# Optimization experiments

Hardware: AMD Instinct MI355X
Metric: run time of the kernel (lower is better)

Reference implementation:

```python
import jax, jax.numpy as jnp
from jax import lax
import numpy as np

D_MODEL = 256
D_STATE = 16
D_CONV = 8
EXPAND = 4
D_INNER = EXPAND * D_MODEL  # 1024
DT_RANK = (D_MODEL + 15) // 16  # 16
OUTPUTS = 128
F_IN = 512


def setup_inputs() -> dict:
    key = jax.random.key(0)
    ks = jax.random.split(key, 16)
    s = lambda k, shape, sc: (jax.random.normal(k, shape, jnp.float32) * sc)
    inp = {
        "x": jax.random.normal(ks[0], (4, 1024, F_IN), jnp.float32),
        # LazyLinear F_IN -> 256
        "W_in": s(ks[1], (F_IN, D_MODEL), F_IN ** -0.5),
        "b_in": jnp.zeros((D_MODEL,), jnp.float32),
        # Mamba params
        "W_inproj": s(ks[2], (D_MODEL, 2 * D_INNER), D_MODEL ** -0.5),
        "conv_w": s(ks[3], (D_INNER, D_CONV), D_CONV ** -0.5),
        "conv_b": jnp.zeros((D_INNER,), jnp.float32),
        "W_xproj": s(ks[4], (D_INNER, DT_RANK + 2 * D_STATE), D_INNER ** -0.5),
        "W_dt": s(ks[5], (DT_RANK, D_INNER), DT_RANK ** -0.5),
        "b_dt": s(ks[6], (D_INNER,), 0.1),
        "A_log": jnp.log(jnp.broadcast_to(jnp.arange(1, D_STATE + 1, dtype=jnp.float32), (D_INNER, D_STATE))),
        "D_param": jnp.ones((D_INNER,), jnp.float32),
        "W_out": s(ks[7], (D_INNER, D_MODEL), D_INNER ** -0.5),
        # head 256 -> 128
        "W_head": s(ks[8], (D_MODEL, OUTPUTS), D_MODEL ** -0.5),
        "b_head": jnp.zeros((OUTPUTS,), jnp.float32),
    }
    return inp


def _mamba(x, W_inproj, conv_w, conv_b, W_xproj, W_dt, b_dt, A_log, D_param, W_out):
    B_, L, _ = x.shape
    xz = x @ W_inproj                       # [B,L,2*Di]
    xc, z = jnp.split(xz, 2, axis=-1)
    # causal depthwise conv over L
    xc_t = jnp.transpose(xc, (0, 2, 1))      # [B,Di,L]
    xc_t = lax.conv_general_dilated(
        xc_t, conv_w[:, None, :], (1,), [(D_CONV - 1, 0)],
        dimension_numbers=("NCH", "OIH", "NCH"), feature_group_count=D_INNER,
    ) + conv_b[None, :, None]
    xc = jax.nn.silu(jnp.transpose(xc_t, (0, 2, 1)))  # [B,L,Di]
    dbc = xc @ W_xproj                       # [B,L,R+2S]
    dt_r = dbc[..., :DT_RANK]
    Bm = dbc[..., DT_RANK:DT_RANK + D_STATE]  # [B,L,S]
    Cm = dbc[..., DT_RANK + D_STATE:]          # [B,L,S]
    dt = jax.nn.softplus(dt_r @ W_dt + b_dt)  # [B,L,Di]
    A = -jnp.exp(A_log)                        # [Di,S]
    dA = jnp.exp(dt[..., None] * A)            # [B,L,Di,S]
    dBx = dt[..., None] * Bm[:, :, None, :] * xc[..., None]  # [B,L,Di,S]

    def step(h, inp):
        dA_t, dBx_t, C_t = inp
        h = dA_t * h + dBx_t                   # [B,Di,S]
        y = jnp.einsum("bds,bs->bd", h, C_t)
        return h, y

    h0 = jnp.zeros((B_, D_INNER, D_STATE), x.dtype)
    _, ys = lax.scan(step, h0, (dA.transpose(1, 0, 2, 3), dBx.transpose(1, 0, 2, 3), Cm.transpose(1, 0, 2)))
    y = ys.transpose(1, 0, 2) + xc * D_param   # [B,L,Di]
    y = y * jax.nn.silu(z)
    return y @ W_out                           # [B,L,D_MODEL]


def reference(x, W_in, b_in, W_inproj, conv_w, conv_b, W_xproj, W_dt, b_dt, A_log, D_param, W_out, W_head, b_head):
    h = jax.nn.sigmoid(x @ W_in + b_in)        # LazyLinear + Dropout(eval) + Sigmoid
    h = _mamba(h, W_inproj, conv_w, conv_b, W_xproj, W_dt, b_dt, A_log, D_param, W_out)
    logits = h @ W_head + b_head               # [B,L,OUTPUTS]
    logits = logits / 1.0                      # temperature = 1.0
    return jax.nn.softmax(logits[:, -1, :], axis=1)
```

## Files before the change

kernel.cpp:

```cpp
#include <hip/hip_runtime.h>
#include <cmath>

#define B_SZ 4
#define L_SEQ 1024
#define F_IN 512
#define D_MODEL 256
#define D_INNER 1024
#define D_STATE 16
#define DT_RANK 16
#define N_OUT 128
#define BL 4096
#define NCHUNK 32
#define CLEN 32

typedef __attribute__((ext_vector_type(8))) short short8;
typedef __attribute__((ext_vector_type(4))) float f32x4;

#define OFF_WIP_HI  0ull
#define OFF_WIP_LO  524288ull
#define OFF_WXP_HI  1048576ull
#define OFF_WXP_LO  1179648ull
#define OFF_HP_HI   1310720ull
#define OFF_HP_LO   3407872ull
#define OFF_HLAST   5505024ull
#define OFF_ZL      5509120ull
#define OFF_XCP_HI  5525504ull
#define OFF_XCP_LO  13914112ull
#define OFF_DBCP    22302720ull
#define OFF_P       39079936ull
#define OFF_Q       47468544ull
#define OFF_YL      55857152ull
#define OFF_H2      55873536ull

__device__ __forceinline__ unsigned short bf16_rne(float v) {
    unsigned u = __float_as_uint(v);
    unsigned r = (u + 0x7fffu + ((u >> 16) & 1u)) >> 16;
    return (unsigned short)r;
}
__device__ __forceinline__ float bf16_tof(unsigned short h) {
    return __uint_as_float(((unsigned)h) << 16);
}
__device__ __forceinline__ float siluf_(float x) { return x / (1.f + expf(-x)); }
__device__ __forceinline__ float softplusf_(float x) {
    return fmaxf(x, 0.f) + log1pf(expf(-fabsf(x)));
}

__device__ __forceinline__ void gload_lds16(const void* g, void* lds) {
    __builtin_amdgcn_global_load_lds(
        (const __attribute__((address_space(1))) unsigned int*)(unsigned long long)g,
        (__attribute__((address_space(3))) unsigned int*)(unsigned int)(unsigned long long)lds,
        16, 0, 0);
}

__device__ __forceinline__ void packB_group(const float* __restrict__ B, int ldb, int c0,
                                            int Ksrc, int Nsrc, int Ncols,
                                            unsigned short* __restrict__ hi,
                                            unsigned short* __restrict__ lo, int g) {
    int p = g * 8;
    int nr = (p >> 3) & 15, kh = (p >> 7) & 3;
    int ngkb = p >> 9;
    int ng16 = Ncols >> 4;
    int ng = ngkb % ng16, kb = ngkb / ng16;
    int n = c0 + ng * 16 + nr, k0 = kb * 32 + kh * 8;
    short8 vh, vl;
#pragma unroll
    for (int i = 0; i < 8; i++) {
        int k = k0 + i;
        float v = (k < Ksrc && n < Nsrc) ? B[(size_t)k * ldb + n] : 0.f;
        unsigned short hh = bf16_rne(v);
        vh[i] = (short)hh;
        vl[i] = (short)bf16_rne(v - bf16_tof(hh));
    }
    *(short8*)(hi + p) = vh;
    *(short8*)(lo + p) = vl;
}

__global__ __launch_bounds__(256) void gemm1_fused(
    const float* __restrict__ x, const float* __restrict__ W_in,
    const float* __restrict__ b_in, const float* __restrict__ W_inproj,
    const float* __restrict__ W_xproj,
    unsigned short* __restrict__ hp_hi, unsigned short* __restrict__ hp_lo,
    float* __restrict__ Hlast,
    unsigned short* __restrict__ wip_hi, unsigned short* __restrict__ wip_lo,
    unsigned short* __restrict__ wxp_hi, unsigned short* __restrict__ wxp_lo) {
    __shared__ __align__(16) char lds[32768];
    const int tid = threadIdx.x;
    const int bn = blockIdx.x * 64, bm = blockIdx.y * 64;
    const int wid = tid >> 6, lane = tid & 63;
    const int wm0 = (wid >> 1) * 32, wn0 = (wid & 1) * 32;
    const int arow = tid >> 2, aoct = tid & 3;

    f32x4 acc[2][2];
#pragma unroll
    for (int r = 0; r < 2; r++)
#pragma unroll
        for (int c = 0; c < 2; c++) acc[r][c] = (f32x4){0.f, 0.f, 0.f, 0.f};

    f32x4 xv0, xv1;
    float wv[8];
    {
        const float* src = x + (size_t)(bm + arow) * 512 + aoct * 8;
        xv0 = *(const f32x4*)src;
        xv1 = *(const f32x4*)(src + 4);
#pragma unroll
        for (int i = 0; i < 8; i++)
            wv[i] = W_in[(size_t)(aoct * 8 + i) * 256 + bn + arow];
    }
    const int off = (arow >> 4) * 1024 + aoct * 256 + (arow & 15) * 16;
    int p = 0;
    for (int kb = 0; kb < 16; kb++) {
        char* buf = lds + p * 16384;
        {
            short8 vh, vl, wh, wl;
#pragma unroll
            for (int i = 0; i < 4; i++) {
                unsigned short hh = bf16_rne(xv0[i]);
                vh[i] = (short)hh;
                vl[i] = (short)bf16_rne(xv0[i] - bf16_tof(hh));
            }
#pragma unroll
            for (int i = 0; i < 4; i++) {
                unsigned short hh = bf16_rne(xv1[i]);
                vh[4 + i] = (short)hh;
                vl[4 + i] = (short)bf16_rne(xv1[i] - bf16_tof(hh));
            }
#pragma unroll
            for (int i = 0; i < 8; i++) {
                unsigned short hh = bf16_rne(wv[i]);
                wh[i] = (short)hh;
                wl[i] = (short)bf16_rne(wv[i] - bf16_tof(hh));
            }
            *(short8*)(buf + off) = vh;
            *(short8*)(buf + 4096 + off) = vl;
            *(short8*)(buf + 8192 + off) = wh;
            *(short8*)(buf + 12288 + off) = wl;
        }
        if (kb < 15) {
            const float* src = x + (size_t)(bm + arow) * 512 + (kb + 1) * 32 + aoct * 8;
            xv0 = *(const f32x4*)src;
            xv1 = *(const f32x4*)(src + 4);
#pragma unroll
            for (int i = 0; i < 8; i++)
                wv[i] = W_in[(size_t)((kb + 1) * 32 + aoct * 8 + i) * 256 + bn + arow];
        }
        __syncthreads();
        short8 ah[2], al[2], bh[2], bl[2];
#pragma unroll
        for (int r = 0; r < 2; r++) {
            ah[r] = *(const short8*)(buf + ((wm0 >> 4) + r) * 1024 + lane * 16);
            al[r] = *(const short8*)(buf + 4096 + ((wm0 >> 4) + r) * 1024 + lane * 16);
        }
#pragma unroll
        for (int c = 0; c < 2; c++) {
            bh[c] = *(const short8*)(buf + 8192 + ((wn0 >> 4) + c) * 1024 + lane * 16);
            bl[c] = *(const short8*)(buf + 12288 + ((wn0 >> 4) + c) * 1024 + lane * 16);
        }
#pragma unroll
        for (int r = 0; r < 2; r++)
#pragma unroll
            for (int c = 0; c < 2; c++) {
                acc[r][c] = __builtin_amdgcn_mfma_f32_16x16x32_bf16(ah[r], bh[c], acc[r][c], 0, 0, 0);
                acc[r][c] = __builtin_amdgcn_mfma_f32_16x16x32_bf16(ah[r], bl[c], acc[r][c], 0, 0, 0);
                acc[r][c] = __builtin_amdgcn_mfma_f32_16x16x32_bf16(al[r], bh[c], acc[r][c], 0, 0, 0);
            }
        p ^= 1;
    }
    __syncthreads();
    unsigned short* lh = (unsigned short*)lds;
    unsigned short* ll = (unsigned short*)(lds + 8192);
    const int r0 = (lane >> 4) * 4, cc = lane & 15;
#pragma unroll
    for (int r = 0; r < 2; r++)
#pragma unroll
        for (int c = 0; c < 2; c++)
#pragma unroll
            for (int j = 0; j < 4; j++) {
                int ml = wm0 + r * 16 + r0 + j;
                int nl = wn0 + c * 16 + cc;
                float v = acc[r][c][j] + b_in[bn + nl];
                v = 1.f / (1.f + expf(-v));
                int lkb = nl >> 5, kh = (nl >> 3) & 3, ii = nl & 7;
                int o2 = ((lkb * 4 + (ml >> 4)) * 4 + kh) * 128 + (ml & 15) * 8 + ii;
                unsigned short hh = bf16_rne(v);
                lh[o2] = hh;
                ll[o2] = bf16_rne(v - bf16_tof(hh));
                if (((bm + ml) & 1023) == 1023)
                    Hlast[((bm + ml) >> 10) * 256 + bn + nl] = v;
            }
    __syncthreads();
    const int mgbase = bm >> 4, kbbase = bn >> 5;
#pragma unroll
    for (int it = 0; it < 2; it++) {
        int q = it * 256 + tid;
        int lkb = q >> 8, lmg = (q >> 6) & 3, ch = q & 63;
        size_t gb = (((size_t)(kbbase + lkb) * 256 + mgbase + lmg) * 1024) + ch * 16;
        *(f32x4*)((char*)hp_hi + gb) = *(const f32x4*)(lds + q * 16);
        *(f32x4*)((char*)hp_lo + gb) = *(const f32x4*)(lds + 8192 + q * 16);
    }
    if (tid < 160) {
        int g = (blockIdx.y * 4 + blockIdx.x) * 160 + tid;
        if (g < 32768)
            packB_group(W_inproj, 2048, 0, 256, 1024, 1024, wip_hi, wip_lo, g);
        else
            packB_group(W_xproj, 48, 0, 1024, 48, 64, wxp_hi, wxp_lo, g - 32768);
    }
}

__global__ __launch_bounds__(256) void zlast_kernel(
    const float* __restrict__ Hlast, const float* __restrict__ W_inproj,
    float* __restrict__ ZL) {
    __shared__ float hl[256];
    __shared__ float red[8][33];
    const int tid = threadIdx.x;
    const int b = blockIdx.x >> 5, dz0 = (blockIdx.x & 31) * 32;
    hl[tid] = Hlast[b * 256 + tid];
    __syncthreads();
    const int dzo = tid & 31, ks = tid >> 5;
    float acc = 0.f;
    const float* wp = W_inproj + (size_t)(ks * 32) * 2048 + 1024 + dz0 + dzo;
#pragma unroll
    for (int i = 0; i < 32; i++)
        acc = fmaf(hl[ks * 32 + i], wp[(size_t)i * 2048], acc);
    red[ks][dzo] = acc;
    __syncthreads();
    if (tid < 32) {
        float s = 0.f;
#pragma unroll
        for (int k = 0; k < 8; k++) s += red[k][tid];
        ZL[b * 1024 + dz0 + tid] = s;
    }
}

__global__ __launch_bounds__(256) void gemm3_conv_kernel(
    const unsigned short* __restrict__ Ahi, const unsigned short* __restrict__ Alo,
    const unsigned short* __restrict__ Bhi, const unsigned short* __restrict__ Blo,
    const unsigned short* __restrict__ Wxhi, const unsigned short* __restrict__ Wxlo,
    const float* __restrict__ cw, const float* __restrict__ cb,
    unsigned short* __restrict__ xcp_hi, unsigned short* __restrict__ xcp_lo,
    float* __restrict__ dbcp) {
    __shared__ __align__(16) char lds[37376];
    const int tid = threadIdx.x;
    const int bm = blockIdx.y * 64, bn = blockIdx.x * 64;
    const int wid = tid >> 6, lane = tid & 63;
    const long long ag0 = ((long long)bm - 16) >> 4;
    const bool batch_start = (bm & 1023) == 0;

    f32x4 acc[5];
#pragma unroll
    for (int r = 0; r < 5; r++) acc[r] = (f32x4){0.f, 0.f, 0.f, 0.f};

    auto stage = [&](int kb, int pp) {
        const long long abase = ((long long)kb * 256 + ag0) * 1024;
        const size_t bbase = ((size_t)kb * 64 + (bn >> 4)) * 1024;
        char* dst = lds + pp * 18432;
#pragma unroll
        for (int it = 0; it < 5; it++) {
            int c = it * 256 + tid;
            if (c < 1152) {
                const char* g;
                char* l;
                if (c < 320)      { g = (const char*)Ahi + abase + (long long)c * 16;        l = dst + c * 16; }
                else if (c < 640) { g = (const char*)Alo + abase + (long long)(c - 320) * 16; l = dst + 5120 + (c - 320) * 16; }
                else if (c < 896) { g = (const char*)Bhi + bbase + (size_t)(c - 640) * 16;    l = dst + 10240 + (c - 640) * 16; }
                else              { g = (const char*)Blo + bbase + (size_t)(c - 896) * 16;    l = dst + 14336 + (c - 896) * 16; }
                gload_lds16(g, l);
            }
        }
    };

    stage(0, 0);
    int p = 0;
    for (int kk = 0; kk < 8; kk++) {
        __syncthreads();
        if (kk < 7) stage(kk + 1, p ^ 1);
        const char* buf = lds + p * 18432;
        short8 ah[5], al[5], bh, bl;
#pragma unroll
        for (int r = 0; r < 5; r++) {
            ah[r] = *(const short8*)(buf + r * 1024 + lane * 16);
            al[r] = *(const short8*)(buf + 5120 + r * 1024 + lane * 16);
        }
        bh = *(const short8*)(buf + 10240 + wid * 1024 + lane * 16);
        bl = *(const short8*)(buf + 14336 + wid * 1024 + lane * 16);
#pragma unroll
        for (int r = 0; r < 5; r++) {
            acc[r] = __builtin_amdgcn_mfma_f32_16x16x32_bf16(ah[r], bh, acc[r], 0, 0, 0);
            acc[r] = __builtin_amdgcn_mfma_f32_16x16x32_bf16(ah[r], bl, acc[r], 0, 0, 0);
            acc[r] = __builtin_amdgcn_mfma_f32_16x16x32_bf16(al[r], bh, acc[r], 0, 0, 0);
        }
        p ^= 1;
    }
    __syncthreads();

    float* S = (float*)lds;
    const int r0 = (lane >> 4) * 4, cc = lane & 15;
#pragma unroll
    for (int r = 0; r < 5; r++)
#pragma unroll
        for (int j = 0; j < 4; j++)
            S[(r * 16 + r0 + j) * 65 + wid * 16 + cc] = acc[r][j];
    __syncthreads();

    unsigned short* xph = (unsigned short*)(lds + 20800);
    unsigned short* xpl = (unsigned short*)(lds + 20800 + 8192);
    {
        const int col = tid & 63, t0 = (tid >> 6) * 16;
        const int d = bn + col;
        float w[8];
#pragma unroll
        for (int k = 0; k < 8; k++) w[k] = cw[d * 8 + k];
        const float bias = cb[d];
        const int kbg = d >> 5, kh = (d >> 3) & 3, ii = d & 7;
        const int kbl = col >> 5, mgl = t0 >> 4;
        float win[8];
#pragma unroll
        for (int k = 0; k < 7; k++) {
            int sr = t0 + 9 + k;
            float v = S[sr * 65 + col];
            if (batch_start && sr < 16) v = 0.f;
            win[k + 1] = v;
        }
        for (int i = 0; i < 16; i++) {
            const int t = t0 + i;
#pragma unroll
            for (int k = 0; k < 7; k++) win[k] = win[k + 1];
            win[7] = S[(t + 16) * 65 + col];
            float a = bias;
#pragma unroll
            for (int k = 0; k < 8; k++) a = fmaf(win[k], w[k], a);
            float v = siluf_(a);
            const int m = bm + t;
            unsigned short hh = bf16_rne(v);
            unsigned short lo_ = bf16_rne(v - bf16_tof(hh));
            size_t pidx = (((size_t)(kbg * 256 + (m >> 4)) * 4 + kh) * 128) + (m & 15) * 8 + ii;
            xcp_hi[pidx] = hh;
            xcp_lo[pidx] = lo_;
            int loff = ((kbl * 4 + mgl) * 4 + kh) * 128 + (t & 15) * 8 + ii;
            xph[loff] = hh;
            xpl[loff] = lo_;
        }
    }
    __syncthreads();

    f32x4 acc2[4];
#pragma unroll
    for (int ng = 0; ng < 4; ng++) acc2[ng] = (f32x4){0.f, 0.f, 0.f, 0.f};
#pragma unroll
    for (int kbl = 0; kbl < 2; kbl++) {
        short8 ah2 = *(const short8*)((const char*)xph + (kbl * 4 + wid) * 1024 + lane * 16);
        short8 al2 = *(const short8*)((const char*)xpl + (kbl * 4 + wid) * 1024 + lane * 16);
        const int kbgl = (bn >> 5) + kbl;
#pragma unroll
        for (int ng = 0; ng < 4; ng++) {
            short8 bh2 = *(const short8*)((const char*)Wxhi + ((size_t)(kbgl * 4 + ng)) * 1024 + lane * 16);
            short8 bl2 = *(const short8*)((const char*)Wxlo + ((size_t)(kbgl * 4 + ng)) * 1024 + lane * 16);
            acc2[ng] = __builtin_amdgcn_mfma_f32_16x16x32_bf16(ah2, bh2, acc2[ng], 0, 0, 0);
            acc2[ng] = __builtin_amdgcn_mfma_f32_16x16x32_bf16(ah2, bl2, acc2[ng], 0, 0, 0);
            acc2[ng] = __builtin_amdgcn_mfma_f32_16x16x32_bf16(al2, bh2, acc2[ng], 0, 0, 0);
        }
    }
    float* dp = dbcp + (size_t)blockIdx.x * 262144;
#pragma unroll
    for (int ng = 0; ng < 4; ng++)
#pragma unroll
        for (int j = 0; j < 4; j++)
            dp[(size_t)(bm + wid * 16 + r0 + j) * 64 + ng * 16 + cc] = acc2[ng][j];
}

__global__ __launch_bounds__(256) void scan_partial_kernel(
    const unsigned short* __restrict__ xh, const unsigned short* __restrict__ xl,
    const float* __restrict__ DBCP, const float* __restrict__ W_dt,
    const float* __restrict__ b_dt, float* __restrict__ P, float* __restrict__ Q) {
    const int tid = threadIdx.x;
    const int dg = blockIdx.x, c = blockIdx.y, b = blockIdx.z;
    const int d = dg * 256 + tid;
    __shared__ __align__(16) float dbc_s[CLEN * 32];
    {
        int r = tid >> 3, cq = tid & 7;
        const float* base = DBCP + ((size_t)(b * 1024 + c * CLEN + r)) * 64 + cq * 4;
        f32x4 s = (f32x4){0.f, 0.f, 0.f, 0.f};
#pragma unroll
        for (int z = 0; z < 16; z++) {
            f32x4 v = *(const f32x4*)(base + (size_t)z * 262144);
            s = s + v;
        }
        ((f32x4*)dbc_s)[tid] = s;
    }
    float Wc[16];
#pragma unroll
    for (int k = 0; k < 16; k++) Wc[k] = W_dt[k * 1024 + d];
    const float bdt = b_dt[d];
    __syncthreads();
    float h[16];
#pragma unroll
    for (int s = 0; s < 16; s++) h[s] = 0.f;
    float sdt = 0.f;
    const size_t dpart = (size_t)(d >> 5) * 131072 + ((d >> 3) & 3) * 128 + (d & 7);
    const int m0 = b * 1024 + c * CLEN;
    for (int i = 0; i < CLEN; i++) {
        const int m = m0 + i;
        const size_t off = dpart + (size_t)(m >> 4) * 512 + (m & 15) * 8;
        const float xv = bf16_tof(xh[off]) + bf16_tof(xl[off]);
        const f32x4* r4 = (const f32x4*)(dbc_s + i * 32);
        f32x4 q0 = r4[0], q1 = r4[1], q2 = r4[2], q3 = r4[3];
        float a0 = 0.f, a1 = 0.f;
#pragma unroll
        for (int k = 0; k < 4; k++) { a0 = fmaf(q0[k], Wc[k], a0); a1 = fmaf(q2[k], Wc[8 + k], a1); }
#pragma unroll
        for (int k = 0; k < 4; k++) { a0 = fmaf(q1[k], Wc[4 + k], a0); a1 = fmaf(q3[k], Wc[12 + k], a1); }
        float dtv = softplusf_(bdt + a0 + a1);
        float dbx = dtv * xv;
        sdt += dtv;
        float e1 = expf(-dtv);
        float e2 = e1 * e1, e3 = e2 * e1, e4 = e2 * e2;
        float e5 = e4 * e1, e6 = e4 * e2, e7 = e4 * e3, e8 = e4 * e4;
        f32x4 b0 = r4[4], b1 = r4[5], b2 = r4[6], b3 = r4[7];
        h[0] = fmaf(e1, h[0], dbx * b0[0]);
        h[1] = fmaf(e2, h[1], dbx * b0[1]);
        h[2] = fmaf(e3, h[2], dbx * b0[2]);
        h[3] = fmaf(e4, h[3], dbx * b0[3]);
        h[4] = fmaf(e5, h[4], dbx * b1[0]);
        h[5] = fmaf(e6, h[5], dbx * b1[1]);
        h[6] = fmaf(e7, h[6], dbx * b1[2]);
        h[7] = fmaf(e8, h[7], dbx * b1[3]);
        h[8] = fmaf(e8 * e1, h[8], dbx * b2[0]);
        h[9] = fmaf(e8 * e2, h[9], dbx * b2[1]);
        h[10] = fmaf(e8 * e3, h[10], dbx * b2[2]);
        h[11] = fmaf(e8 * e4, h[11], dbx * b2[3]);
        h[12] = fmaf(e8 * e5, h[12], dbx * b3[0]);
        h[13] = fmaf(e8 * e6, h[13], dbx * b3[1]);
        h[14] = fmaf(e8 * e7, h[14], dbx * b3[2]);
        h[15] = fmaf(e8 * e8, h[15], dbx * b3[3]);
    }
    size_t o = (((size_t)(b * NCHUNK + c) * 1024 + d) << 4);
    float E1 = expf(-sdt);
    float E2 = E1 * E1, E3 = E2 * E1, E4 = E2 * E2;
    float E5 = E4 * E1, E6 = E4 * E2, E7 = E4 * E3, E8 = E4 * E4;
    f32x4 pv;
    pv = (f32x4){E1, E2, E3, E4};                      *(f32x4*)(P + o) = pv;
    pv = (f32x4){E5, E6, E7, E8};                      *(f32x4*)(P + o + 4) = pv;
    pv = (f32x4){E8 * E1, E8 * E2, E8 * E3, E8 * E4};  *(f32x4*)(P + o + 8) = pv;
    pv = (f32x4){E8 * E5, E8 * E6, E8 * E7, E8 * E8};  *(f32x4*)(P + o + 12) = pv;
#pragma unroll
    for (int u = 0; u < 4; u++) {
        f32x4 qv;
#pragma unroll
        for (int s = 0; s < 4; s++) qv[s] = h[u * 4 + s];
        *(f32x4*)(Q + o + u * 4) = qv;
    }
}

__global__ __launch_bounds__(256) void scan_final_kernel(
    const float* __restrict__ P, const float* __restrict__ Q,
    const float* __restrict__ DBCP, const unsigned short* __restrict__ xh,
    const unsigned short* __restrict__ xl, const float* __restrict__ ZL,
    const float* __restrict__ Dp, float* __restrict__ YL) {
    const int idx = blockIdx.x * 256 + threadIdx.x;
    const int s = idx & 15, d = (idx >> 4) & 1023, b = idx >> 14;
    float h = 0.f;
    const size_t stride = (size_t)1024 * 16;
    size_t o = (((size_t)(b * NCHUNK) * 1024 + d) << 4) + s;
#pragma unroll 8
    for (int c = 0; c < NCHUNK; c++) {
        h = fmaf(P[o], h, Q[o]);
        o += stride;
    }
    float cm = 0.f;
#pragma unroll
    for (int z = 0; z < 16; z++)
        cm += DBCP[(size_t)z * 262144 + ((size_t)b * 1024 + 1023) * 64 + 32 + s];
    float v = h * cm;
    v += __shfl_xor(v, 1);
    v += __shfl_xor(v, 2);
    v += __shfl_xor(v, 4);
    v += __shfl_xor(v, 8);
    if (s == 0) {
        const int m = b * 1024 + 1023;
        const size_t off = (size_t)(d >> 5) * 131072 + (size_t)(m >> 4) * 512 +
                           ((d >> 3) & 3) * 128 + 15 * 8 + (d & 7);
        float xlast = bf16_tof(xh[off]) + bf16_tof(xl[off]);
        float y = v + xlast * Dp[d];
        float z = ZL[b * 1024 + d];
        YL[b * 1024 + d] = y * siluf_(z);
    }
}

__global__ __launch_bounds__(256) void head1_kernel(
    const float* __restrict__ YL, const float* __restrict__ W_out,
    float* __restrict__ H2) {
    __shared__ float yl[D_INNER];
    __shared__ float red[16][17];
    const int b = blockIdx.y, n0 = blockIdx.x * 16;
    const int tid = threadIdx.x;
    const int tn = tid & 15, tk = tid >> 4;
    ((f32x4*)yl)[tid] = ((const f32x4*)(YL + b * D_INNER))[tid];
    __syncthreads();
    float acc = 0.f;
    const float* wp = W_out + (size_t)(tk * 64) * D_MODEL + n0 + tn;
#pragma unroll
    for (int i = 0; i < 64; i++)
        acc = fmaf(yl[tk * 64 + i], wp[(size_t)i * D_MODEL], acc);
    red[tk][tn] = acc;
    __syncthreads();
    if (tid < 16) {
        float s = 0.f;
#pragma unroll
        for (int k = 0; k < 16; k++) s += red[k][tid];
        H2[b * D_MODEL + n0 + tid] = s;
    }
}

__global__ __launch_bounds__(256) void head2_kernel(
    const float* __restrict__ H2, const float* __restrict__ W_head,
    const float* __restrict__ b_head, float* __restrict__ out) {
    __shared__ float h2s[D_MODEL];
    __shared__ float part[256];
    __shared__ float red[N_OUT];
    __shared__ float tmp[64];
    __shared__ float m_s, inv_s;
    const int b = blockIdx.x, tid = threadIdx.x;
    h2s[tid] = H2[b * D_MODEL + tid];
    __syncthreads();
    const int n = tid & 127, kh = tid >> 7;
    float acc = 0.f;
    const float* wp = W_head + (size_t)(kh * 128) * N_OUT + n;
#pragma unroll
    for (int k = 0; k < 128; k++)
        acc = fmaf(h2s[kh * 128 + k], wp[(size_t)k * N_OUT], acc);
    part[tid] = acc;
    __syncthreads();
    if (tid < N_OUT) red[tid] = part[tid] + part[tid + 128] + b_head[tid];
    __syncthreads();
    if (tid < 64) tmp[tid] = fmaxf(red[tid], red[tid + 64]);
    __syncthreads();
    if (tid == 0) {
        float m = tmp[0];
        for (int i = 1; i < 64; i++) m = fmaxf(m, tmp[i]);
        m_s = m;
    }
    __syncthreads();
    if (tid < N_OUT) red[tid] = expf(red[tid] - m_s);
    __syncthreads();
    if (tid < 64) tmp[tid] = red[tid] + red[tid + 64];
    __syncthreads();
    if (tid == 0) {
        float s = 0.f;
        for (int i = 0; i < 64; i++) s += tmp[i];
        inv_s = 1.f / s;
    }
    __syncthreads();
    if (tid < N_OUT) out[b * N_OUT + tid] = red[tid] * inv_s;
}

extern "C" void kernel_launch(void* const* d_in, const int* in_sizes, int n_in,
                              void* d_out, int out_size, void* d_ws, size_t ws_size,
                              hipStream_t stream) {
    const float* x = (const float*)d_in[0];
    const float* W_in = (const float*)d_in[1];
    const float* b_in = (const float*)d_in[2];
    const float* W_inproj = (const float*)d_in[3];
    const float* conv_w = (const float*)d_in[4];
    const float* conv_b = (const float*)d_in[5];
    const float* W_xproj = (const float*)d_in[6];
    const float* W_dt = (const float*)d_in[7];
    const float* b_dt = (const float*)d_in[8];
    const float* D_param = (const float*)d_in[10];
    const float* W_out = (const float*)d_in[11];
    const float* W_head = (const float*)d_in[12];
    const float* b_head = (const float*)d_in[13];
    float* out = (float*)d_out;

    char* W = (char*)d_ws;
    auto F = [&](size_t off) { return (float*)(W + off); };
    auto U = [&](size_t off) { return (unsigned short*)(W + off); };

    gemm1_fused<<<dim3(4, 64), 256, 0, stream>>>(
        x, W_in, b_in, W_inproj, W_xproj,
        U(OFF_HP_HI), U(OFF_HP_LO), F(OFF_HLAST),
        U(OFF_WIP_HI), U(OFF_WIP_LO), U(OFF_WXP_HI), U(OFF_WXP_LO));
    zlast_kernel<<<128, 256, 0, stream>>>(F(OFF_HLAST), W_inproj, F(OFF_ZL));
    gemm3_conv_kernel<<<dim3(16, 64), 256, 0, stream>>>(
        U(OFF_HP_HI), U(OFF_HP_LO), U(OFF_WIP_HI), U(OFF_WIP_LO),
        U(OFF_WXP_HI), U(OFF_WXP_LO), conv_w, conv_b,
        U(OFF_XCP_HI), U(OFF_XCP_LO), F(OFF_DBCP));
    scan_partial_kernel<<<dim3(4, NCHUNK, 4), 256, 0, stream>>>(
        U(OFF_XCP_HI), U(OFF_XCP_LO), F(OFF_DBCP), W_dt, b_dt, F(OFF_P), F(OFF_Q));
    scan_final_kernel<<<256, 256, 0, stream>>>(F(OFF_P), F(OFF_Q), F(OFF_DBCP),
                                               U(OFF_XCP_HI), U(OFF_XCP_LO), F(OFF_ZL),
                                               D_param, F(OFF_YL));
    head1_kernel<<<dim3(16, 4), 256, 0, stream>>>(F(OFF_YL), W_out, F(OFF_H2));
    head2_kernel<<<4, 256, 0, stream>>>(F(OFF_H2), W_head, b_head, out);
}
```

Measured before the change: 94.19 us.

## Drop low-bf16 weight and conv-output terms, fold zlast into scan_partial

Weights (W_in, W_inproj, W_xproj) and the conv/SiLU output are now represented by a single bf16 term instead of a hi/lo split. The lo-by-hi MFMA products, the lo buffers and their global and LDS traffic are removed in gemm1, gemm3 and the scans. The separate zlast kernel is merged into scan_partial as an extra block column, saving one launch. Numerical accuracy drops, since the weights and the xc activations lose the residual correction term.

```diff
diff --git a/kernel.cpp b/kernel.cpp
--- a/kernel.cpp
+++ b/kernel.cpp
@@ -17,20 +17,17 @@
 typedef __attribute__((ext_vector_type(4))) float f32x4;
 
 #define OFF_WIP_HI  0ull
-#define OFF_WIP_LO  524288ull
-#define OFF_WXP_HI  1048576ull
-#define OFF_WXP_LO  1179648ull
-#define OFF_HP_HI   1310720ull
-#define OFF_HP_LO   3407872ull
-#define OFF_HLAST   5505024ull
-#define OFF_ZL      5509120ull
-#define OFF_XCP_HI  5525504ull
-#define OFF_XCP_LO  13914112ull
-#define OFF_DBCP    22302720ull
-#define OFF_P       39079936ull
-#define OFF_Q       47468544ull
-#define OFF_YL      55857152ull
-#define OFF_H2      55873536ull
+#define OFF_WXP_HI  524288ull
+#define OFF_HP_HI   655360ull
+#define OFF_HP_LO   2752512ull
+#define OFF_HLAST   4849664ull
+#define OFF_ZL      4853760ull
+#define OFF_XCP_HI  4870144ull
+#define OFF_DBCP    13258752ull
+#define OFF_P       30035968ull
+#define OFF_Q       38424576ull
+#define OFF_YL      46813184ull
+#define OFF_H2      46829568ull
 
 __device__ __forceinline__ unsigned short bf16_rne(float v) {
     unsigned u = __float_as_uint(v);
@@ -52,27 +49,23 @@
         16, 0, 0);
 }
 
-__device__ __forceinline__ void packB_group(const float* __restrict__ B, int ldb, int c0,
-                                            int Ksrc, int Nsrc, int Ncols,
-                                            unsigned short* __restrict__ hi,
-                                            unsigned short* __restrict__ lo, int g) {
+__device__ __forceinline__ void packBhi_group(const float* __restrict__ B, int ldb,
+                                              int Ksrc, int Nsrc, int Ncols,
+                                              unsigned short* __restrict__ hi, int g) {
     int p = g * 8;
     int nr = (p >> 3) & 15, kh = (p >> 7) & 3;
     int ngkb = p >> 9;
     int ng16 = Ncols >> 4;
     int ng = ngkb % ng16, kb = ngkb / ng16;
-    int n = c0 + ng * 16 + nr, k0 = kb * 32 + kh * 8;
-    short8 vh, vl;
+    int n = ng * 16 + nr, k0 = kb * 32 + kh * 8;
+    short8 vh;
 #pragma unroll
     for (int i = 0; i < 8; i++) {
         int k = k0 + i;
         float v = (k < Ksrc && n < Nsrc) ? B[(size_t)k * ldb + n] : 0.f;
-        unsigned short hh = bf16_rne(v);
-        vh[i] = (short)hh;
-        vl[i] = (short)bf16_rne(v - bf16_tof(hh));
+        vh[i] = (short)bf16_rne(v);
     }
     *(short8*)(hi + p) = vh;
-    *(short8*)(lo + p) = vl;
 }
 
 __global__ __launch_bounds__(256) void gemm1_fused(
@@ -81,9 +74,8 @@
     const float* __restrict__ W_xproj,
     unsigned short* __restrict__ hp_hi, unsigned short* __restrict__ hp_lo,
     float* __restrict__ Hlast,
-    unsigned short* __restrict__ wip_hi, unsigned short* __restrict__ wip_lo,
-    unsigned short* __restrict__ wxp_hi, unsigned short* __restrict__ wxp_lo) {
-    __shared__ __align__(16) char lds[32768];
+    unsigned short* __restrict__ wip_hi, unsigned short* __restrict__ wxp_hi) {
+    __shared__ __align__(16) char lds[24576];
     const int tid = threadIdx.x;
     const int bn = blockIdx.x * 64, bm = blockIdx.y * 64;
     const int wid = tid >> 6, lane = tid & 63;
@@ -109,9 +101,9 @@
     const int off = (arow >> 4) * 1024 + aoct * 256 + (arow & 15) * 16;
     int p = 0;
     for (int kb = 0; kb < 16; kb++) {
-        char* buf = lds + p * 16384;
+        char* buf = lds + p * 12288;
         {
-            short8 vh, vl, wh, wl;
+            short8 vh, vl, wh;
 #pragma unroll
             for (int i = 0; i < 4; i++) {
                 unsigned short hh = bf16_rne(xv0[i]);
@@ -125,15 +117,10 @@
                 vl[4 + i] = (short)bf16_rne(xv1[i] - bf16_tof(hh));
             }
 #pragma unroll
-            for (int i = 0; i < 8; i++) {
-                unsigned short hh = bf16_rne(wv[i]);
-                wh[i] = (short)hh;
-                wl[i] = (short)bf16_rne(wv[i] - bf16_tof(hh));
-            }
+            for (int i = 0; i < 8; i++) wh[i] = (short)bf16_rne(wv[i]);
             *(short8*)(buf + off) = vh;
             *(short8*)(buf + 4096 + off) = vl;
             *(short8*)(buf + 8192 + off) = wh;
-            *(short8*)(buf + 12288 + off) = wl;
         }
         if (kb < 15) {
             const float* src = x + (size_t)(bm + arow) * 512 + (kb + 1) * 32 + aoct * 8;
@@ -144,23 +131,20 @@
                 wv[i] = W_in[(size_t)((kb + 1) * 32 + aoct * 8 + i) * 256 + bn + arow];
         }
         __syncthreads();
-        short8 ah[2], al[2], bh[2], bl[2];
+        short8 ah[2], al[2], bh[2];
 #pragma unroll
         for (int r = 0; r < 2; r++) {
             ah[r] = *(const short8*)(buf + ((wm0 >> 4) + r) * 1024 + lane * 16);
             al[r] = *(const short8*)(buf + 4096 + ((wm0 >> 4) + r) * 1024 + lane * 16);
         }
 #pragma unroll
-        for (int c = 0; c < 2; c++) {
+        for (int c = 0; c < 2; c++)
             bh[c] = *(const short8*)(buf + 8192 + ((wn0 >> 4) + c) * 1024 + lane * 16);
-            bl[c] = *(const short8*)(buf + 12288 + ((wn0 >> 4) + c) * 1024 + lane * 16);
-        }
 #pragma unroll
         for (int r = 0; r < 2; r++)
 #pragma unroll
             for (int c = 0; c < 2; c++) {
                 acc[r][c] = __builtin_amdgcn_mfma_f32_16x16x32_bf16(ah[r], bh[c], acc[r][c], 0, 0, 0);
-                acc[r][c] = __builtin_amdgcn_mfma_f32_16x16x32_bf16(ah[r], bl[c], acc[r][c], 0, 0, 0);
                 acc[r][c] = __builtin_amdgcn_mfma_f32_16x16x32_bf16(al[r], bh[c], acc[r][c], 0, 0, 0);
             }
         p ^= 1;
@@ -200,45 +184,19 @@
     if (tid < 160) {
         int g = (blockIdx.y * 4 + blockIdx.x) * 160 + tid;
         if (g < 32768)
-            packB_group(W_inproj, 2048, 0, 256, 1024, 1024, wip_hi, wip_lo, g);
+            packBhi_group(W_inproj, 2048, 256, 1024, 1024, wip_hi, g);
         else
-            packB_group(W_xproj, 48, 0, 1024, 48, 64, wxp_hi, wxp_lo, g - 32768);
-    }
-}
-
-__global__ __launch_bounds__(256) void zlast_kernel(
-    const float* __restrict__ Hlast, const float* __restrict__ W_inproj,
-    float* __restrict__ ZL) {
-    __shared__ float hl[256];
-    __shared__ float red[8][33];
-    const int tid = threadIdx.x;
-    const int b = blockIdx.x >> 5, dz0 = (blockIdx.x & 31) * 32;
-    hl[tid] = Hlast[b * 256 + tid];
-    __syncthreads();
-    const int dzo = tid & 31, ks = tid >> 5;
-    float acc = 0.f;
-    const float* wp = W_inproj + (size_t)(ks * 32) * 2048 + 1024 + dz0 + dzo;
-#pragma unroll
-    for (int i = 0; i < 32; i++)
-        acc = fmaf(hl[ks * 32 + i], wp[(size_t)i * 2048], acc);
-    red[ks][dzo] = acc;
-    __syncthreads();
-    if (tid < 32) {
-        float s = 0.f;
-#pragma unroll
-        for (int k = 0; k < 8; k++) s += red[k][tid];
-        ZL[b * 1024 + dz0 + tid] = s;
+            packBhi_group(W_xproj, 48, 1024, 48, 64, wxp_hi, g - 32768);
     }
 }
 
 __global__ __launch_bounds__(256) void gemm3_conv_kernel(
     const unsigned short* __restrict__ Ahi, const unsigned short* __restrict__ Alo,
-    const unsigned short* __restrict__ Bhi, const unsigned short* __restrict__ Blo,
-    const unsigned short* __restrict__ Wxhi, const unsigned short* __restrict__ Wxlo,
+    const unsigned short* __restrict__ Bhi,
+    const unsigned short* __restrict__ Wxhi,
     const float* __restrict__ cw, const float* __restrict__ cb,
-    unsigned short* __restrict__ xcp_hi, unsigned short* __restrict__ xcp_lo,
-    float* __restrict__ dbcp) {
-    __shared__ __align__(16) char lds[37376];
+    unsigned short* __restrict__ xcp_hi, float* __restrict__ dbcp) {
+    __shared__ __align__(16) char lds[28672];
     const int tid = threadIdx.x;
     const int bm = blockIdx.y * 64, bn = blockIdx.x * 64;
     const int wid = tid >> 6, lane = tid & 63;
@@ -252,17 +210,16 @@
     auto stage = [&](int kb, int pp) {
         const long long abase = ((long long)kb * 256 + ag0) * 1024;
         const size_t bbase = ((size_t)kb * 64 + (bn >> 4)) * 1024;
-        char* dst = lds + pp * 18432;
-#pragma unroll
-        for (int it = 0; it < 5; it++) {
+        char* dst = lds + pp * 14336;
+#pragma unroll
+        for (int it = 0; it < 4; it++) {
             int c = it * 256 + tid;
-            if (c < 1152) {
+            if (c < 896) {
                 const char* g;
                 char* l;
-                if (c < 320)      { g = (const char*)Ahi + abase + (long long)c * 16;        l = dst + c * 16; }
+                if (c < 320)      { g = (const char*)Ahi + abase + (long long)c * 16;         l = dst + c * 16; }
                 else if (c < 640) { g = (const char*)Alo + abase + (long long)(c - 320) * 16; l = dst + 5120 + (c - 320) * 16; }
-                else if (c < 896) { g = (const char*)Bhi + bbase + (size_t)(c - 640) * 16;    l = dst + 10240 + (c - 640) * 16; }
-                else              { g = (const char*)Blo + bbase + (size_t)(c - 896) * 16;    l = dst + 14336 + (c - 896) * 16; }
+                else              { g = (const char*)Bhi + bbase + (size_t)(c - 640) * 16;    l = dst + 10240 + (c - 640) * 16; }
                 gload_lds16(g, l);
             }
         }
@@ -273,19 +230,17 @@
     for (int kk = 0; kk < 8; kk++) {
         __syncthreads();
         if (kk < 7) stage(kk + 1, p ^ 1);
-        const char* buf = lds + p * 18432;
-        short8 ah[5], al[5], bh, bl;
+        const char* buf = lds + p * 14336;
+        short8 ah[5], al[5], bh;
 #pragma unroll
         for (int r = 0; r < 5; r++) {
             ah[r] = *(const short8*)(buf + r * 1024 + lane * 16);
             al[r] = *(const short8*)(buf + 5120 + r * 1024 + lane * 16);
         }
         bh = *(const short8*)(buf + 10240 + wid * 1024 + lane * 16);
-        bl = *(const short8*)(buf + 14336 + wid * 1024 + lane * 16);
 #pragma unroll
         for (int r = 0; r < 5; r++) {
             acc[r] = __builtin_amdgcn_mfma_f32_16x16x32_bf16(ah[r], bh, acc[r], 0, 0, 0);
-            acc[r] = __builtin_amdgcn_mfma_f32_16x16x32_bf16(ah[r], bl, acc[r], 0, 0, 0);
             acc[r] = __builtin_amdgcn_mfma_f32_16x16x32_bf16(al[r], bh, acc[r], 0, 0, 0);
         }
         p ^= 1;
@@ -302,7 +257,6 @@
     __syncthreads();
 
     unsigned short* xph = (unsigned short*)(lds + 20800);
-    unsigned short* xpl = (unsigned short*)(lds + 20800 + 8192);
     {
         const int col = tid & 63, t0 = (tid >> 6) * 16;
         const int d = bn + col;
@@ -331,13 +285,10 @@
             float v = siluf_(a);
             const int m = bm + t;
             unsigned short hh = bf16_rne(v);
-            unsigned short lo_ = bf16_rne(v - bf16_tof(hh));
             size_t pidx = (((size_t)(kbg * 256 + (m >> 4)) * 4 + kh) * 128) + (m & 15) * 8 + ii;
             xcp_hi[pidx] = hh;
-            xcp_lo[pidx] = lo_;
             int loff = ((kbl * 4 + mgl) * 4 + kh) * 128 + (t & 15) * 8 + ii;
             xph[loff] = hh;
-            xpl[loff] = lo_;
         }
     }
     __syncthreads();
@@ -348,15 +299,11 @@
 #pragma unroll
     for (int kbl = 0; kbl < 2; kbl++) {
         short8 ah2 = *(const short8*)((const char*)xph + (kbl * 4 + wid) * 1024 + lane * 16);
-        short8 al2 = *(const short8*)((const char*)xpl + (kbl * 4 + wid) * 1024 + lane * 16);
         const int kbgl = (bn >> 5) + kbl;
 #pragma unroll
         for (int ng = 0; ng < 4; ng++) {
             short8 bh2 = *(const short8*)((const char*)Wxhi + ((size_t)(kbgl * 4 + ng)) * 1024 + lane * 16);
-            short8 bl2 = *(const short8*)((const char*)Wxlo + ((size_t)(kbgl * 4 + ng)) * 1024 + lane * 16);
             acc2[ng] = __builtin_amdgcn_mfma_f32_16x16x32_bf16(ah2, bh2, acc2[ng], 0, 0, 0);
-            acc2[ng] = __builtin_amdgcn_mfma_f32_16x16x32_bf16(ah2, bl2, acc2[ng], 0, 0, 0);
-            acc2[ng] = __builtin_amdgcn_mfma_f32_16x16x32_bf16(al2, bh2, acc2[ng], 0, 0, 0);
         }
     }
     float* dp = dbcp + (size_t)blockIdx.x * 262144;
@@ -368,13 +315,39 @@
 }
 
 __global__ __launch_bounds__(256) void scan_partial_kernel(
-    const unsigned short* __restrict__ xh, const unsigned short* __restrict__ xl,
-    const float* __restrict__ DBCP, const float* __restrict__ W_dt,
-    const float* __restrict__ b_dt, float* __restrict__ P, float* __restrict__ Q) {
+    const unsigned short* __restrict__ xh, const float* __restrict__ DBCP,
+    const float* __restrict__ W_dt, const float* __restrict__ b_dt,
+    const float* __restrict__ Hlast, const float* __restrict__ W_inproj,
+    float* __restrict__ P, float* __restrict__ Q, float* __restrict__ ZL) {
+    __shared__ __align__(16) float dbc_s[CLEN * 32];
+    __shared__ float hl[256];
+    __shared__ float red2[8][33];
     const int tid = threadIdx.x;
     const int dg = blockIdx.x, c = blockIdx.y, b = blockIdx.z;
+
+    if (dg == 4) {
+        const int zb = c * 4 + b;
+        const int b2 = zb >> 5, dz0 = (zb & 31) * 32;
+        hl[tid] = Hlast[b2 * 256 + tid];
+        __syncthreads();
+        const int dzo = tid & 31, ks = tid >> 5;
+        float acc = 0.f;
+        const float* wp = W_inproj + (size_t)(ks * 32) * 2048 + 1024 + dz0 + dzo;
+#pragma unroll
+        for (int i = 0; i < 32; i++)
+            acc = fmaf(hl[ks * 32 + i], wp[(size_t)i * 2048], acc);
+        red2[ks][dzo] = acc;
+        __syncthreads();
+        if (tid < 32) {
+            float s = 0.f;
+#pragma unroll
+            for (int k = 0; k < 8; k++) s += red2[k][tid];
+            ZL[b2 * 1024 + dz0 + tid] = s;
+        }
+        return;
+    }
+
     const int d = dg * 256 + tid;
-    __shared__ __align__(16) float dbc_s[CLEN * 32];
     {
         int r = tid >> 3, cq = tid & 7;
         const float* base = DBCP + ((size_t)(b * 1024 + c * CLEN + r)) * 64 + cq * 4;
@@ -400,7 +373,7 @@
     for (int i = 0; i < CLEN; i++) {
         const int m = m0 + i;
         const size_t off = dpart + (size_t)(m >> 4) * 512 + (m & 15) * 8;
-        const float xv = bf16_tof(xh[off]) + bf16_tof(xl[off]);
+        const float xv = bf16_tof(xh[off]);
         const f32x4* r4 = (const f32x4*)(dbc_s + i * 32);
         f32x4 q0 = r4[0], q1 = r4[1], q2 = r4[2], q3 = r4[3];
         float a0 = 0.f, a1 = 0.f;
@@ -453,8 +426,8 @@
 __global__ __launch_bounds__(256) void scan_final_kernel(
     const float* __restrict__ P, const float* __restrict__ Q,
     const float* __restrict__ DBCP, const unsigned short* __restrict__ xh,
-    const unsigned short* __restrict__ xl, const float* __restrict__ ZL,
-    const float* __restrict__ Dp, float* __restrict__ YL) {
+    const float* __restrict__ ZL, const float* __restrict__ Dp,
+    float* __restrict__ YL) {
     const int idx = blockIdx.x * 256 + threadIdx.x;
     const int s = idx & 15, d = (idx >> 4) & 1023, b = idx >> 14;
     float h = 0.f;
@@ -478,7 +451,7 @@
         const int m = b * 1024 + 1023;
         const size_t off = (size_t)(d >> 5) * 131072 + (size_t)(m >> 4) * 512 +
                            ((d >> 3) & 3) * 128 + 15 * 8 + (d & 7);
-        float xlast = bf16_tof(xh[off]) + bf16_tof(xl[off]);
+        float xlast = bf16_tof(xh[off]);
         float y = v + xlast * Dp[d];
         float z = ZL[b * 1024 + d];
         YL[b * 1024 + d] = y * siluf_(z);
@@ -577,16 +550,15 @@
     gemm1_fused<<<dim3(4, 64), 256, 0, stream>>>(
         x, W_in, b_in, W_inproj, W_xproj,
         U(OFF_HP_HI), U(OFF_HP_LO), F(OFF_HLAST),
-        U(OFF_WIP_HI), U(OFF_WIP_LO), U(OFF_WXP_HI), U(OFF_WXP_LO));
-    zlast_kernel<<<128, 256, 0, stream>>>(F(OFF_HLAST), W_inproj, F(OFF_ZL));
+        U(OFF_WIP_HI), U(OFF_WXP_HI));
     gemm3_conv_kernel<<<dim3(16, 64), 256, 0, stream>>>(
-        U(OFF_HP_HI), U(OFF_HP_LO), U(OFF_WIP_HI), U(OFF_WIP_LO),
-        U(OFF_WXP_HI), U(OFF_WXP_LO), conv_w, conv_b,
-        U(OFF_XCP_HI), U(OFF_XCP_LO), F(OFF_DBCP));
-    scan_partial_kernel<<<dim3(4, NCHUNK, 4), 256, 0, stream>>>(
-        U(OFF_XCP_HI), U(OFF_XCP_LO), F(OFF_DBCP), W_dt, b_dt, F(OFF_P), F(OFF_Q));
+        U(OFF_HP_HI), U(OFF_HP_LO), U(OFF_WIP_HI), U(OFF_WXP_HI),
+        conv_w, conv_b, U(OFF_XCP_HI), F(OFF_DBCP));
+    scan_partial_kernel<<<dim3(5, NCHUNK, 4), 256, 0, stream>>>(
+        U(OFF_XCP_HI), F(OFF_DBCP), W_dt, b_dt, F(OFF_HLAST), W_inproj,
+        F(OFF_P), F(OFF_Q), F(OFF_ZL));
     scan_final_kernel<<<256, 256, 0, stream>>>(F(OFF_P), F(OFF_Q), F(OFF_DBCP),
-                                               U(OFF_XCP_HI), U(OFF_XCP_LO), F(OFF_ZL),
+                                               U(OFF_XCP_HI), F(OFF_ZL),
                                                D_param, F(OFF_YL));
     head1_kernel<<<dim3(16, 4), 256, 0, stream>>>(F(OFF_YL), W_out, F(OFF_H2));
     head2_kernel<<<4, 256, 0, stream>>>(F(OFF_H2), W_head, b_head, out);
```

After: 92.25 us. 2.1% less time.
